# Performance work log

Measured on AMD Instinct MI355X. Metric: run time of the kernel, lower is better.

Reference implementation:

```python
import jax, jax.numpy as jnp
import numpy as np

N_BATCH = 4096
D_FEAT = 64
N_CLASSES = 10
DET_EPS = 1e-8


def setup_inputs() -> dict:
    key = jax.random.key(0)
    k1, k2, k3 = jax.random.split(key, 3)
    # small-magnitude means and variances bounded away from 0 keep the
    # KL values (and hence sigmoid(KL)) in a numerically meaningful range
    mu = jax.random.normal(k1, (N_BATCH, D_FEAT), dtype=jnp.float32) * 0.1
    var = jax.random.uniform(k2, (N_BATCH, D_FEAT), dtype=jnp.float32) + 0.5
    labels = jax.random.randint(k3, (N_BATCH,), 0, N_CLASSES)
    return {"mu": mu, "var": var, "labels": labels}


def _pairwise_kl(mu, var):
    """K[i, j] = KL(N(mu_i, diag(var_i)) || N(mu_j, diag(var_j))),
    matching the original's kl_mvn on the row/col tiling, but computed
    elementwise/matmul instead of dense diag_embed + inv/det (same math:
    inv(diag(S1)) @ diag(S0) summed == sum(S0/S1); det(diag(S)) == prod(S))."""
    D = mu.shape[1]
    inv_var = 1.0 / var                                   # [N, D]
    # tr term: sum_d var_i,d / var_j,d
    tr = var @ inv_var.T                                  # [N, N]
    # det term: det(S1)/ (det(S0)+eps) with diagonal determinants = products
    p = jnp.prod(var, axis=1)                             # [N]
    det = p[None, :] / (p[:, None] + DET_EPS)             # [N, N]
    # quad term: sum_d (mu_j - mu_i)^2 / var_j,d, expanded into matmuls
    mu_sq = mu * mu                                       # [N, D]
    quad = (mu_sq @ inv_var.T
            - 2.0 * (mu @ (mu * inv_var).T)
            + jnp.sum(mu_sq * inv_var, axis=1)[None, :])  # [N, N]
    return 0.5 * (tr + det + quad - D)


def reference(mu, var, labels):
    N = mu.shape[0]
    K = _pairwise_kl(mu, var)                 # KL(i -> j)
    sym = 0.5 * (K + K.T)                     # symmetric_kl over the pair grid
    logits = jax.nn.sigmoid(sym)              # [N, N]

    same = labels[:, None] == labels[None, :]
    off_diag = ~jnp.eye(N, dtype=bool)        # logits_mask: zero out diagonal
    p_mask = (same & off_diag).astype(logits.dtype)
    n_mask = ((~same) & off_diag).astype(logits.dtype)

    pos = logits * p_mask
    neg = logits * n_mask
    return (jnp.mean(pos), jnp.mean(neg), jnp.sum(pos), jnp.sum(neg))
```

## Files before the change

kernel.cpp:

```cpp
#include <hip/hip_runtime.h>


#define N 4096
#define D 64
#define KH 256
#define MT 128
#define TILES2 32
#define NBLK2 528
#define DET_EPS 1e-8f

typedef short bf16x8 __attribute__((ext_vector_type(8)));
typedef float f32x16 __attribute__((ext_vector_type(16)));

#define WS_H    0
#define WS_PSL  (N * KH * 2)
#define WS_PART (WS_PSL + N * 16)

static __device__ __forceinline__ unsigned short f2bf(float x) {
  unsigned int u = __float_as_uint(x);
  unsigned int r = (u + 0x7FFFu + ((u >> 16) & 1u)) >> 16;
  return (unsigned short)r;
}

static __device__ __forceinline__ f32x16 mfma_bf16(bf16x8 a, bf16x8 b, f32x16 c) {
  return __builtin_amdgcn_mfma_f32_32x32x16_bf16(a, b, c, 0, 0, 0);
}

__global__ __launch_bounds__(256) void precompute_kernel(
    const float* __restrict__ mu, const float* __restrict__ var,
    const int* __restrict__ labels,
    unsigned short* __restrict__ Hf, float4* __restrict__ PSL) {
  const int t = threadIdx.x;
  const int lane = t & 63;
  const int w = t >> 6;
  const int r = blockIdx.x * 4 + w;

  const float m = mu[r * D + lane];
  const float v = var[r * D + lane];
  const float g0 = 1.0f / v;
  const float f0 = v + m * m;
  const float f1 = -2.0f * m;
  const float g1 = m * g0;

  const size_t base = (size_t)(r >> 5) * 8192 + (size_t)(lane >> 2) * 512
                      + (size_t)(r & 31) * 16 + (size_t)(lane & 3) * 4;
  *(ushort4*)&Hf[base] = make_ushort4(f2bf(f0), f2bf(f1), f2bf(g0), f2bf(g1));

  float p = v;
  float s = m * m * g0;
  #pragma unroll
  for (int off = 1; off < 64; off <<= 1) {
    p *= __shfl_xor(p, off);
    s += __shfl_xor(s, off);
  }
  if (lane == 0) {
    PSL[r] = make_float4(p, 1.0f / (p + DET_EPS), 0.25f * s - 16.0f,
                         (float)labels[r]);
  }
}

__global__ __launch_bounds__(256, 2) void pair_kernel(
    const unsigned short* __restrict__ Hf,
    const float4* __restrict__ PSL, float* __restrict__ partial) {
  __shared__ float4 sPi[128];
  __shared__ float4 sPj[128];
  __shared__ float red[8];

  int L = (int)blockIdx.x;
  int it = (int)(32.5f - sqrtf(32.5f * 32.5f - 2.0f * (float)L));
  while (it > 0 && L < it * TILES2 - it * (it - 1) / 2) --it;
  while (L >= (it + 1) * TILES2 - (it + 1) * it / 2) ++it;
  const int jt = it + (L - (it * TILES2 - it * (it - 1) / 2));
  const int i0 = it * MT, j0 = jt * MT;

  const int t = threadIdx.x;
  const int lane = t & 63;
  const int w = t >> 6;
  const int sr = w >> 1, sc = w & 1;

  if (t < 128) sPi[t] = PSL[i0 + t];
  else sPj[t - 128] = PSL[j0 + t - 128];
  __syncthreads();

  const int l31 = lane & 31;
  const int slot = l31 * 16 + (lane >> 5) * 8;
  const unsigned short* pa = Hf + (size_t)(i0 / 32 + sr * 2) * 8192 + slot;
  const unsigned short* pb = Hf + (size_t)(j0 / 32 + sc * 2) * 8192 + slot;

  const bool active = !(it == jt && w == 2);

  f32x16 C00 = {}, C01 = {}, C10 = {}, C11 = {};
  float pos = 0.0f, neg = 0.0f;

  if (active) {
    #pragma unroll 4
    for (int k = 0; k < 16; ++k) {
      const bf16x8 a0 = *(const bf16x8*)(pa + k * 512);
      const bf16x8 a1 = *(const bf16x8*)(pa + 8192 + k * 512);
      const bf16x8 c0 = *(const bf16x8*)(pb + k * 512);
      const bf16x8 c1 = *(const bf16x8*)(pb + 8192 + k * 512);
      const bf16x8 b0 = __builtin_shufflevector(c0, c0, 2, 3, 0, 1, 6, 7, 4, 5);
      const bf16x8 b1 = __builtin_shufflevector(c1, c1, 2, 3, 0, 1, 6, 7, 4, 5);
      C00 = mfma_bf16(a0, b0, C00);
      C01 = mfma_bf16(a0, b1, C01);
      C10 = mfma_bf16(a1, b0, C10);
      C11 = mfma_bf16(a1, b1, C11);
    }

    const int rbase = 4 * (lane >> 5);
    #pragma unroll
    for (int mn = 0; mn < 4; ++mn) {
      const int m = mn >> 1, n = mn & 1;
      const f32x16 C = (mn == 0) ? C00 : (mn == 1) ? C01 : (mn == 2) ? C10 : C11;
      const int jloc = (sc * 2 + n) * 32 + l31;
      const int j = j0 + jloc;
      const float4 pj = sPj[jloc];
      #pragma unroll
      for (int r = 0; r < 16; ++r) {
        const int row = (r & 3) + 8 * (r >> 2) + rbase;
        const int iloc = (sr * 2 + m) * 32 + row;
        const int i = i0 + iloc;
        if (i < j) {
          const float4 pi = sPi[iloc];
          const float det = pj.x * pi.y + pi.x * pj.y;
          const float sym = 0.25f * (C[r] + det) + pi.z + pj.z;
          const float sig = __builtin_amdgcn_rcpf(1.0f + __expf(-sym));
          if (pi.w == pj.w) pos += sig; else neg += sig;
        }
      }
    }
  }

  #pragma unroll
  for (int off = 32; off > 0; off >>= 1) {
    pos += __shfl_down(pos, off);
    neg += __shfl_down(neg, off);
  }
  if (lane == 0) { red[w] = pos; red[4 + w] = neg; }
  __syncthreads();
  if (t == 0) {
    partial[L]         = red[0] + red[1] + red[2] + red[3];
    partial[NBLK2 + L] = red[4] + red[5] + red[6] + red[7];
  }
}

__global__ __launch_bounds__(256) void finalize_kernel(
    const float* __restrict__ partial, float* __restrict__ out) {
  __shared__ float redp[4], redn[4];
  const int t = threadIdx.x;
  const int lane = t & 63, w = t >> 6;
  float p = 0.0f, n = 0.0f;
  for (int i = t; i < NBLK2; i += 256) {
    p += partial[i];
    n += partial[NBLK2 + i];
  }
  #pragma unroll
  for (int off = 32; off > 0; off >>= 1) {
    p += __shfl_down(p, off);
    n += __shfl_down(n, off);
  }
  if (lane == 0) { redp[w] = p; redn[w] = n; }
  __syncthreads();
  if (t == 0) {
    const float pos = 2.0f * (redp[0] + redp[1] + redp[2] + redp[3]);
    const float neg = 2.0f * (redn[0] + redn[1] + redn[2] + redn[3]);
    out[0] = pos * (1.0f / 16777216.0f);
    out[1] = neg * (1.0f / 16777216.0f);
    out[2] = pos;
    out[3] = neg;
  }
}

extern "C" void kernel_launch(void* const* d_in, const int* in_sizes, int n_in,
                              void* d_out, int out_size, void* d_ws, size_t ws_size,
                              hipStream_t stream) {
  const float* mu = (const float*)d_in[0];
  const float* var = (const float*)d_in[1];
  const int* labels = (const int*)d_in[2];
  float* out = (float*)d_out;
  char* ws = (char*)d_ws;

  unsigned short* Hf = (unsigned short*)(ws + WS_H);
  float4* PSL = (float4*)(ws + WS_PSL);
  float* partial = (float*)(ws + WS_PART);

  precompute_kernel<<<dim3(N / 4), dim3(256), 0, stream>>>(mu, var, labels, Hf, PSL);
  pair_kernel<<<dim3(NBLK2), dim3(256), 0, stream>>>(Hf, PSL, partial);
  finalize_kernel<<<dim3(1), dim3(256), 0, stream>>>(partial, out);
}
```

Measured before the change: 78.68 us.

## Fuse precompute, pair and finalize into one cooperative kernel with grid syncs

Replaces the three launches with a single cooperative kernel of 512 blocks. Each block precomputes 8 rows, grid-syncs, then processes one off-diagonal tile or two diagonal tiles, grid-syncs again, and block 0 does the final reduction. The aim is to remove launch gaps and inter-kernel overhead, at the cost of two grid-wide barriers and some load imbalance, since the blocks that take two diagonal tiles do less work per tile. The original three-kernel path stays as a fallback if the cooperative launch fails.

```diff
diff --git a/kernel.cpp b/kernel.cpp
--- a/kernel.cpp
+++ b/kernel.cpp
@@ -1,4 +1,7 @@
 #include <hip/hip_runtime.h>
+#include <hip/hip_cooperative_groups.h>
+
+namespace cg = cooperative_groups;
 
 
 #define N 4096
@@ -6,7 +9,9 @@
 #define KH 256
 #define MT 128
 #define TILES2 32
+#define NOFF 496
 #define NBLK2 528
+#define GRID1 512
 #define DET_EPS 1e-8f
 
 typedef short bf16x8 __attribute__((ext_vector_type(8)));
@@ -26,15 +31,10 @@
   return __builtin_amdgcn_mfma_f32_32x32x16_bf16(a, b, c, 0, 0, 0);
 }
 
-__global__ __launch_bounds__(256) void precompute_kernel(
-    const float* __restrict__ mu, const float* __restrict__ var,
+static __device__ __forceinline__ void row_precompute(
+    int r, int lane, const float* __restrict__ mu, const float* __restrict__ var,
     const int* __restrict__ labels,
     unsigned short* __restrict__ Hf, float4* __restrict__ PSL) {
-  const int t = threadIdx.x;
-  const int lane = t & 63;
-  const int w = t >> 6;
-  const int r = blockIdx.x * 4 + w;
-
   const float m = mu[r * D + lane];
   const float v = var[r * D + lane];
   const float g0 = 1.0f / v;
@@ -59,33 +59,29 @@
   }
 }
 
-__global__ __launch_bounds__(256, 2) void pair_kernel(
+static __device__ __forceinline__ void do_tile(
+    int it, int jt, int slot,
     const unsigned short* __restrict__ Hf,
     const float4* __restrict__ PSL, float* __restrict__ partial) {
   __shared__ float4 sPi[128];
   __shared__ float4 sPj[128];
   __shared__ float red[8];
 
-  int L = (int)blockIdx.x;
-  int it = (int)(32.5f - sqrtf(32.5f * 32.5f - 2.0f * (float)L));
-  while (it > 0 && L < it * TILES2 - it * (it - 1) / 2) --it;
-  while (L >= (it + 1) * TILES2 - (it + 1) * it / 2) ++it;
-  const int jt = it + (L - (it * TILES2 - it * (it - 1) / 2));
   const int i0 = it * MT, j0 = jt * MT;
-
   const int t = threadIdx.x;
   const int lane = t & 63;
   const int w = t >> 6;
   const int sr = w >> 1, sc = w & 1;
 
+  __syncthreads();
   if (t < 128) sPi[t] = PSL[i0 + t];
   else sPj[t - 128] = PSL[j0 + t - 128];
   __syncthreads();
 
   const int l31 = lane & 31;
-  const int slot = l31 * 16 + (lane >> 5) * 8;
-  const unsigned short* pa = Hf + (size_t)(i0 / 32 + sr * 2) * 8192 + slot;
-  const unsigned short* pb = Hf + (size_t)(j0 / 32 + sc * 2) * 8192 + slot;
+  const int slot_f = l31 * 16 + (lane >> 5) * 8;
+  const unsigned short* pa = Hf + (size_t)(i0 / 32 + sr * 2) * 8192 + slot_f;
+  const unsigned short* pb = Hf + (size_t)(j0 / 32 + sc * 2) * 8192 + slot_f;
 
   const bool active = !(it == jt && w == 2);
 
@@ -139,9 +135,83 @@
   if (lane == 0) { red[w] = pos; red[4 + w] = neg; }
   __syncthreads();
   if (t == 0) {
-    partial[L]         = red[0] + red[1] + red[2] + red[3];
-    partial[NBLK2 + L] = red[4] + red[5] + red[6] + red[7];
-  }
+    partial[slot]         = red[0] + red[1] + red[2] + red[3];
+    partial[NBLK2 + slot] = red[4] + red[5] + red[6] + red[7];
+  }
+}
+
+__global__ __launch_bounds__(256, 2) void fused_kernel(
+    const float* __restrict__ mu, const float* __restrict__ var,
+    const int* __restrict__ labels,
+    unsigned short* __restrict__ Hf, float4* __restrict__ PSL,
+    float* __restrict__ partial, float* __restrict__ out) {
+  const int bid = (int)blockIdx.x;
+  const int t = (int)threadIdx.x;
+  const int lane = t & 63;
+  const int w = t >> 6;
+
+  #pragma unroll
+  for (int itr = 0; itr < 2; ++itr)
+    row_precompute(bid * 8 + itr * 4 + w, lane, mu, var, labels, Hf, PSL);
+
+  cg::this_grid().sync();
+
+  if (bid < NOFF) {
+    int it = (int)((63.0f - sqrtf(3969.0f - 8.0f * (float)bid)) * 0.5f);
+    while (it > 0 && bid < 31 * it - it * (it - 1) / 2) --it;
+    while (bid >= 31 * (it + 1) - (it + 1) * it / 2) ++it;
+    const int jt = it + 1 + (bid - (31 * it - it * (it - 1) / 2));
+    do_tile(it, jt, bid, Hf, PSL, partial);
+  } else {
+    const int dd = bid - NOFF;
+    do_tile(2 * dd,     2 * dd,     NOFF + 2 * dd,     Hf, PSL, partial);
+    do_tile(2 * dd + 1, 2 * dd + 1, NOFF + 2 * dd + 1, Hf, PSL, partial);
+  }
+
+  cg::this_grid().sync();
+
+  if (bid == 0) {
+    __shared__ float redp[4], redn[4];
+    float p = 0.0f, n = 0.0f;
+    for (int i = t; i < NBLK2; i += 256) {
+      p += partial[i];
+      n += partial[NBLK2 + i];
+    }
+    #pragma unroll
+    for (int off = 32; off > 0; off >>= 1) {
+      p += __shfl_down(p, off);
+      n += __shfl_down(n, off);
+    }
+    if (lane == 0) { redp[w] = p; redn[w] = n; }
+    __syncthreads();
+    if (t == 0) {
+      const float pos = 2.0f * (redp[0] + redp[1] + redp[2] + redp[3]);
+      const float neg = 2.0f * (redn[0] + redn[1] + redn[2] + redn[3]);
+      out[0] = pos * (1.0f / 16777216.0f);
+      out[1] = neg * (1.0f / 16777216.0f);
+      out[2] = pos;
+      out[3] = neg;
+    }
+  }
+}
+
+__global__ __launch_bounds__(256) void precompute_kernel(
+    const float* __restrict__ mu, const float* __restrict__ var,
+    const int* __restrict__ labels,
+    unsigned short* __restrict__ Hf, float4* __restrict__ PSL) {
+  const int t = threadIdx.x;
+  row_precompute(blockIdx.x * 4 + (t >> 6), t & 63, mu, var, labels, Hf, PSL);
+}
+
+__global__ __launch_bounds__(256, 2) void pair_kernel(
+    const unsigned short* __restrict__ Hf,
+    const float4* __restrict__ PSL, float* __restrict__ partial) {
+  int L = (int)blockIdx.x;
+  int it = (int)(32.5f - sqrtf(32.5f * 32.5f - 2.0f * (float)L));
+  while (it > 0 && L < it * TILES2 - it * (it - 1) / 2) --it;
+  while (L >= (it + 1) * TILES2 - (it + 1) * it / 2) ++it;
+  const int jt = it + (L - (it * TILES2 - it * (it - 1) / 2));
+  do_tile(it, jt, L, Hf, PSL, partial);
 }
 
 __global__ __launch_bounds__(256) void finalize_kernel(
@@ -184,7 +254,14 @@
   float4* PSL = (float4*)(ws + WS_PSL);
   float* partial = (float*)(ws + WS_PART);
 
-  precompute_kernel<<<dim3(N / 4), dim3(256), 0, stream>>>(mu, var, labels, Hf, PSL);
-  pair_kernel<<<dim3(NBLK2), dim3(256), 0, stream>>>(Hf, PSL, partial);
-  finalize_kernel<<<dim3(1), dim3(256), 0, stream>>>(partial, out);
-}
+  void* args[] = {(void*)&mu, (void*)&var, (void*)&labels,
+                  (void*)&Hf, (void*)&PSL, (void*)&partial, (void*)&out};
+  hipError_t e = hipLaunchCooperativeKernel((const void*)fused_kernel,
+                                            dim3(GRID1), dim3(256), args, 0,
+                                            stream);
+  if (e != hipSuccess) {
+    precompute_kernel<<<dim3(N / 4), dim3(256), 0, stream>>>(mu, var, labels, Hf, PSL);
+    pair_kernel<<<dim3(NBLK2), dim3(256), 0, stream>>>(Hf, PSL, partial);
+    finalize_kernel<<<dim3(1), dim3(256), 0, stream>>>(partial, out);
+  }
+}
```

After: 207.8 us. 164% more time.

## Fuse finalize into pair kernel via last-block reduction and pack diagonal tiles

Applied to the files above, without the earlier changes.

Removes the separate finalize launch: each pair block publishes its partials, bumps an atomic counter reset by the precompute kernel, and the last block to finish does the final reduction. The grid also shrinks from 528 to 512 blocks, with 496 off-diagonal tiles at one per block and the 32 diagonal tiles paired two per block. The diagonal masking becomes a compile-time template specialization. The goal is to drop one launch and even out per-block work, at the cost of atomics, a threadfence, and serial diagonal tiles in the last 16 blocks.

```diff
diff --git a/kernel.cpp b/kernel.cpp
--- a/kernel.cpp
+++ b/kernel.cpp
@@ -6,7 +6,9 @@
 #define KH 256
 #define MT 128
 #define TILES2 32
+#define NOFF 496
 #define NBLK2 528
+#define GRID2 512
 #define DET_EPS 1e-8f
 
 typedef short bf16x8 __attribute__((ext_vector_type(8)));
@@ -15,6 +17,7 @@
 #define WS_H    0
 #define WS_PSL  (N * KH * 2)
 #define WS_PART (WS_PSL + N * 16)
+#define WS_CNT  (WS_PART + 2 * NBLK2 * 4)
 
 static __device__ __forceinline__ unsigned short f2bf(float x) {
   unsigned int u = __float_as_uint(x);
@@ -29,11 +32,14 @@
 __global__ __launch_bounds__(256) void precompute_kernel(
     const float* __restrict__ mu, const float* __restrict__ var,
     const int* __restrict__ labels,
-    unsigned short* __restrict__ Hf, float4* __restrict__ PSL) {
+    unsigned short* __restrict__ Hf, float4* __restrict__ PSL,
+    unsigned int* __restrict__ counter) {
   const int t = threadIdx.x;
   const int lane = t & 63;
   const int w = t >> 6;
   const int r = blockIdx.x * 4 + w;
+
+  if (blockIdx.x == 0 && t == 0) *counter = 0u;
 
   const float m = mu[r * D + lane];
   const float v = var[r * D + lane];
@@ -59,35 +65,29 @@
   }
 }
 
-__global__ __launch_bounds__(256, 2) void pair_kernel(
+template <bool DIAG>
+static __device__ __forceinline__ void do_tile(
+    int it, int jt, int slot,
     const unsigned short* __restrict__ Hf,
-    const float4* __restrict__ PSL, float* __restrict__ partial) {
-  __shared__ float4 sPi[128];
-  __shared__ float4 sPj[128];
-  __shared__ float red[8];
-
-  int L = (int)blockIdx.x;
-  int it = (int)(32.5f - sqrtf(32.5f * 32.5f - 2.0f * (float)L));
-  while (it > 0 && L < it * TILES2 - it * (it - 1) / 2) --it;
-  while (L >= (it + 1) * TILES2 - (it + 1) * it / 2) ++it;
-  const int jt = it + (L - (it * TILES2 - it * (it - 1) / 2));
+    const float4* __restrict__ PSL, float* __restrict__ partial,
+    float4* sPi, float4* sPj, float* red) {
   const int i0 = it * MT, j0 = jt * MT;
-
   const int t = threadIdx.x;
   const int lane = t & 63;
   const int w = t >> 6;
   const int sr = w >> 1, sc = w & 1;
 
+  __syncthreads();
   if (t < 128) sPi[t] = PSL[i0 + t];
   else sPj[t - 128] = PSL[j0 + t - 128];
   __syncthreads();
 
   const int l31 = lane & 31;
-  const int slot = l31 * 16 + (lane >> 5) * 8;
-  const unsigned short* pa = Hf + (size_t)(i0 / 32 + sr * 2) * 8192 + slot;
-  const unsigned short* pb = Hf + (size_t)(j0 / 32 + sc * 2) * 8192 + slot;
-
-  const bool active = !(it == jt && w == 2);
+  const int slot_f = l31 * 16 + (lane >> 5) * 8;
+  const unsigned short* pa = Hf + (size_t)(i0 / 32 + sr * 2) * 8192 + slot_f;
+  const unsigned short* pb = Hf + (size_t)(j0 / 32 + sc * 2) * 8192 + slot_f;
+
+  const bool active = !(DIAG && w == 2);
 
   f32x16 C00 = {}, C01 = {}, C10 = {}, C11 = {};
   float pos = 0.0f, neg = 0.0f;
@@ -113,14 +113,12 @@
       const int m = mn >> 1, n = mn & 1;
       const f32x16 C = (mn == 0) ? C00 : (mn == 1) ? C01 : (mn == 2) ? C10 : C11;
       const int jloc = (sc * 2 + n) * 32 + l31;
-      const int j = j0 + jloc;
       const float4 pj = sPj[jloc];
       #pragma unroll
       for (int r = 0; r < 16; ++r) {
         const int row = (r & 3) + 8 * (r >> 2) + rbase;
         const int iloc = (sr * 2 + m) * 32 + row;
-        const int i = i0 + iloc;
-        if (i < j) {
+        if (!DIAG || (i0 + iloc) < (j0 + jloc)) {
           const float4 pi = sPi[iloc];
           const float det = pj.x * pi.y + pi.x * pj.y;
           const float sym = 0.25f * (C[r] + det) + pi.z + pj.z;
@@ -139,35 +137,63 @@
   if (lane == 0) { red[w] = pos; red[4 + w] = neg; }
   __syncthreads();
   if (t == 0) {
-    partial[L]         = red[0] + red[1] + red[2] + red[3];
-    partial[NBLK2 + L] = red[4] + red[5] + red[6] + red[7];
-  }
-}
-
-__global__ __launch_bounds__(256) void finalize_kernel(
-    const float* __restrict__ partial, float* __restrict__ out) {
-  __shared__ float redp[4], redn[4];
-  const int t = threadIdx.x;
-  const int lane = t & 63, w = t >> 6;
-  float p = 0.0f, n = 0.0f;
-  for (int i = t; i < NBLK2; i += 256) {
-    p += partial[i];
-    n += partial[NBLK2 + i];
-  }
-  #pragma unroll
-  for (int off = 32; off > 0; off >>= 1) {
-    p += __shfl_down(p, off);
-    n += __shfl_down(n, off);
-  }
-  if (lane == 0) { redp[w] = p; redn[w] = n; }
-  __syncthreads();
-  if (t == 0) {
-    const float pos = 2.0f * (redp[0] + redp[1] + redp[2] + redp[3]);
-    const float neg = 2.0f * (redn[0] + redn[1] + redn[2] + redn[3]);
-    out[0] = pos * (1.0f / 16777216.0f);
-    out[1] = neg * (1.0f / 16777216.0f);
-    out[2] = pos;
-    out[3] = neg;
+    atomicExch(&partial[slot],         red[0] + red[1] + red[2] + red[3]);
+    atomicExch(&partial[NBLK2 + slot], red[4] + red[5] + red[6] + red[7]);
+  }
+}
+
+__global__ __launch_bounds__(256, 2) void pair_finalize_kernel(
+    const unsigned short* __restrict__ Hf,
+    const float4* __restrict__ PSL, float* __restrict__ partial,
+    unsigned int* __restrict__ counter, float* __restrict__ out) {
+  __shared__ float4 sPi[128];
+  __shared__ float4 sPj[128];
+  __shared__ float red[8];
+  __shared__ unsigned int sOrd;
+
+  const int bid = (int)blockIdx.x;
+  const int t = (int)threadIdx.x;
+
+  if (bid < NOFF) {
+    int it = (int)((63.0f - sqrtf(3969.0f - 8.0f * (float)bid)) * 0.5f);
+    while (it > 0 && bid < 31 * it - it * (it - 1) / 2) --it;
+    while (bid >= 31 * (it + 1) - (it + 1) * it / 2) ++it;
+    const int jt = it + 1 + (bid - (31 * it - it * (it - 1) / 2));
+    do_tile<false>(it, jt, bid, Hf, PSL, partial, sPi, sPj, red);
+  } else {
+    const int dd = bid - NOFF;
+    do_tile<true>(2 * dd,     2 * dd,     NOFF + 2 * dd,     Hf, PSL, partial,
+                  sPi, sPj, red);
+    do_tile<true>(2 * dd + 1, 2 * dd + 1, NOFF + 2 * dd + 1, Hf, PSL, partial,
+                  sPi, sPj, red);
+  }
+
+  __threadfence();
+  if (t == 0) sOrd = atomicAdd(counter, 1u);
+  __syncthreads();
+  if (sOrd == GRID2 - 1) {
+    __shared__ float redp[4], redn[4];
+    const int lane = t & 63, w = t >> 6;
+    float p = 0.0f, n = 0.0f;
+    for (int i = t; i < NBLK2; i += 256) {
+      p += atomicAdd(&partial[i], 0.0f);
+      n += atomicAdd(&partial[NBLK2 + i], 0.0f);
+    }
+    #pragma unroll
+    for (int off = 32; off > 0; off >>= 1) {
+      p += __shfl_down(p, off);
+      n += __shfl_down(n, off);
+    }
+    if (lane == 0) { redp[w] = p; redn[w] = n; }
+    __syncthreads();
+    if (t == 0) {
+      const float pos = 2.0f * (redp[0] + redp[1] + redp[2] + redp[3]);
+      const float neg = 2.0f * (redn[0] + redn[1] + redn[2] + redn[3]);
+      out[0] = pos * (1.0f / 16777216.0f);
+      out[1] = neg * (1.0f / 16777216.0f);
+      out[2] = pos;
+      out[3] = neg;
+    }
   }
 }
 
@@ -183,8 +209,10 @@
   unsigned short* Hf = (unsigned short*)(ws + WS_H);
   float4* PSL = (float4*)(ws + WS_PSL);
   float* partial = (float*)(ws + WS_PART);
-
-  precompute_kernel<<<dim3(N / 4), dim3(256), 0, stream>>>(mu, var, labels, Hf, PSL);
-  pair_kernel<<<dim3(NBLK2), dim3(256), 0, stream>>>(Hf, PSL, partial);
-  finalize_kernel<<<dim3(1), dim3(256), 0, stream>>>(partial, out);
-}
+  unsigned int* counter = (unsigned int*)(ws + WS_CNT);
+
+  precompute_kernel<<<dim3(N / 4), dim3(256), 0, stream>>>(mu, var, labels, Hf,
+                                                           PSL, counter);
+  pair_finalize_kernel<<<dim3(GRID2), dim3(256), 0, stream>>>(Hf, PSL, partial,
+                                                              counter, out);
+}
```

Result: slower. 107.7 us (+36.9%).

## Switch pair kernel to single-wave 64x64 triangular tiles with prefetched loads

Applied to the files above, without the earlier changes.

Replaces the 256-thread, 128x128 upper-triangle tile blocks with 2080 one-wavefront blocks, each handling a 64x64 tile. Each wave writes its partial sums directly, so the shared-memory cross-wave reduction and its barrier go away. The diagonal-tile masking is specialised via a template, and the k-loop now prefetches the next iteration's operands into registers. The aim is finer load balance across CUs and less idle work on diagonal tiles. The cost is more blocks, more repeated PSL loads, and a larger partial array for finalize to sum.

```diff
diff --git a/kernel.cpp b/kernel.cpp
--- a/kernel.cpp
+++ b/kernel.cpp
@@ -4,9 +4,9 @@
 #define N 4096
 #define D 64
 #define KH 256
-#define MT 128
-#define TILES2 32
-#define NBLK2 528
+#define MT 64
+#define TILES 64
+#define NT 2080
 #define DET_EPS 1e-8f
 
 typedef short bf16x8 __attribute__((ext_vector_type(8)));
@@ -59,74 +59,74 @@
   }
 }
 
-__global__ __launch_bounds__(256, 2) void pair_kernel(
+template <bool DIAG>
+static __device__ __forceinline__ void tile64(
+    int it, int jt, int slot,
     const unsigned short* __restrict__ Hf,
-    const float4* __restrict__ PSL, float* __restrict__ partial) {
-  __shared__ float4 sPi[128];
-  __shared__ float4 sPj[128];
-  __shared__ float red[8];
-
-  int L = (int)blockIdx.x;
-  int it = (int)(32.5f - sqrtf(32.5f * 32.5f - 2.0f * (float)L));
-  while (it > 0 && L < it * TILES2 - it * (it - 1) / 2) --it;
-  while (L >= (it + 1) * TILES2 - (it + 1) * it / 2) ++it;
-  const int jt = it + (L - (it * TILES2 - it * (it - 1) / 2));
+    const float4* __restrict__ PSL, float* __restrict__ partial,
+    float4* sPi, float4* sPj) {
   const int i0 = it * MT, j0 = jt * MT;
-
-  const int t = threadIdx.x;
-  const int lane = t & 63;
-  const int w = t >> 6;
-  const int sr = w >> 1, sc = w & 1;
-
-  if (t < 128) sPi[t] = PSL[i0 + t];
-  else sPj[t - 128] = PSL[j0 + t - 128];
+  const int lane = (int)threadIdx.x & 63;
+  const int l31 = lane & 31;
+
+  sPi[lane] = PSL[i0 + lane];
+  sPj[lane] = PSL[j0 + lane];
   __syncthreads();
 
-  const int l31 = lane & 31;
-  const int slot = l31 * 16 + (lane >> 5) * 8;
-  const unsigned short* pa = Hf + (size_t)(i0 / 32 + sr * 2) * 8192 + slot;
-  const unsigned short* pb = Hf + (size_t)(j0 / 32 + sc * 2) * 8192 + slot;
-
-  const bool active = !(it == jt && w == 2);
+  const int slot_f = l31 * 16 + (lane >> 5) * 8;
+  const unsigned short* pa = Hf + (size_t)(i0 >> 5) * 8192 + slot_f;
+  const unsigned short* pb = Hf + (size_t)(j0 >> 5) * 8192 + slot_f;
+
+#define LDA0(k) (*(const bf16x8*)(pa + (k) * 512))
+#define LDA1(k) (*(const bf16x8*)(pa + 8192 + (k) * 512))
+#define LDB0(k) (*(const bf16x8*)(pb + (k) * 512))
+#define LDB1(k) (*(const bf16x8*)(pb + 8192 + (k) * 512))
+#define PI(x) __builtin_shufflevector((x), (x), 2, 3, 0, 1, 6, 7, 4, 5)
 
   f32x16 C00 = {}, C01 = {}, C10 = {}, C11 = {};
+
+  bf16x8 a0x = LDA0(0), a1x = LDA1(0), b0x = LDB0(0), b1x = LDB1(0);
+  #pragma unroll
+  for (int k = 0; k < 16; ++k) {
+    bf16x8 a0y, a1y, b0y, b1y;
+    if (k < 15) {
+      a0y = LDA0(k + 1); a1y = LDA1(k + 1);
+      b0y = LDB0(k + 1); b1y = LDB1(k + 1);
+    }
+    const bf16x8 p0 = PI(b0x), p1 = PI(b1x);
+    C00 = mfma_bf16(a0x, p0, C00);
+    C01 = mfma_bf16(a0x, p1, C01);
+    C10 = mfma_bf16(a1x, p0, C10);
+    C11 = mfma_bf16(a1x, p1, C11);
+    if (k < 15) {
+      a0x = a0y; a1x = a1y; b0x = b0y; b1x = b1y;
+    }
+  }
+#undef LDA0
+#undef LDA1
+#undef LDB0
+#undef LDB1
+#undef PI
+
+  const int rbase = 4 * (lane >> 5);
   float pos = 0.0f, neg = 0.0f;
-
-  if (active) {
-    #pragma unroll 4
-    for (int k = 0; k < 16; ++k) {
-      const bf16x8 a0 = *(const bf16x8*)(pa + k * 512);
-      const bf16x8 a1 = *(const bf16x8*)(pa + 8192 + k * 512);
-      const bf16x8 c0 = *(const bf16x8*)(pb + k * 512);
-      const bf16x8 c1 = *(const bf16x8*)(pb + 8192 + k * 512);
-      const bf16x8 b0 = __builtin_shufflevector(c0, c0, 2, 3, 0, 1, 6, 7, 4, 5);
-      const bf16x8 b1 = __builtin_shufflevector(c1, c1, 2, 3, 0, 1, 6, 7, 4, 5);
-      C00 = mfma_bf16(a0, b0, C00);
-      C01 = mfma_bf16(a0, b1, C01);
-      C10 = mfma_bf16(a1, b0, C10);
-      C11 = mfma_bf16(a1, b1, C11);
-    }
-
-    const int rbase = 4 * (lane >> 5);
+  #pragma unroll
+  for (int mn = 0; mn < 4; ++mn) {
+    const int m = mn >> 1, n = mn & 1;
+    if (DIAG && m == 1 && n == 0) continue;
+    const f32x16 C = (mn == 0) ? C00 : (mn == 1) ? C01 : (mn == 2) ? C10 : C11;
+    const int jloc = n * 32 + l31;
+    const float4 pj = sPj[jloc];
     #pragma unroll
-    for (int mn = 0; mn < 4; ++mn) {
-      const int m = mn >> 1, n = mn & 1;
-      const f32x16 C = (mn == 0) ? C00 : (mn == 1) ? C01 : (mn == 2) ? C10 : C11;
-      const int jloc = (sc * 2 + n) * 32 + l31;
-      const int j = j0 + jloc;
-      const float4 pj = sPj[jloc];
-      #pragma unroll
-      for (int r = 0; r < 16; ++r) {
-        const int row = (r & 3) + 8 * (r >> 2) + rbase;
-        const int iloc = (sr * 2 + m) * 32 + row;
-        const int i = i0 + iloc;
-        if (i < j) {
-          const float4 pi = sPi[iloc];
-          const float det = pj.x * pi.y + pi.x * pj.y;
-          const float sym = 0.25f * (C[r] + det) + pi.z + pj.z;
-          const float sig = __builtin_amdgcn_rcpf(1.0f + __expf(-sym));
-          if (pi.w == pj.w) pos += sig; else neg += sig;
-        }
+    for (int r = 0; r < 16; ++r) {
+      const int row = (r & 3) + 8 * (r >> 2) + rbase;
+      const int iloc = m * 32 + row;
+      if (!DIAG || (i0 + iloc) < (j0 + jloc)) {
+        const float4 pi = sPi[iloc];
+        const float det = pj.x * pi.y + pi.x * pj.y;
+        const float sym = 0.25f * (C[r] + det) + pi.z + pj.z;
+        const float sig = __builtin_amdgcn_rcpf(1.0f + __expf(-sym));
+        if (pi.w == pj.w) pos += sig; else neg += sig;
       }
     }
   }
@@ -136,12 +136,26 @@
     pos += __shfl_down(pos, off);
     neg += __shfl_down(neg, off);
   }
-  if (lane == 0) { red[w] = pos; red[4 + w] = neg; }
-  __syncthreads();
-  if (t == 0) {
-    partial[L]         = red[0] + red[1] + red[2] + red[3];
-    partial[NBLK2 + L] = red[4] + red[5] + red[6] + red[7];
-  }
+  if (lane == 0) {
+    partial[slot]      = pos;
+    partial[NT + slot] = neg;
+  }
+}
+
+__global__ __launch_bounds__(64, 4) void pair64_kernel(
+    const unsigned short* __restrict__ Hf,
+    const float4* __restrict__ PSL, float* __restrict__ partial) {
+  __shared__ float4 sPi[64];
+  __shared__ float4 sPj[64];
+
+  int L = (int)blockIdx.x;
+  int it = (int)((129.0f - sqrtf(16641.0f - 8.0f * (float)L)) * 0.5f);
+  while (it > 0 && L < it * TILES - it * (it - 1) / 2) --it;
+  while (L >= (it + 1) * TILES - (it + 1) * it / 2) ++it;
+  const int jt = it + (L - (it * TILES - it * (it - 1) / 2));
+
+  if (it == jt) tile64<true>(it, jt, L, Hf, PSL, partial, sPi, sPj);
+  else          tile64<false>(it, jt, L, Hf, PSL, partial, sPi, sPj);
 }
 
 __global__ __launch_bounds__(256) void finalize_kernel(
@@ -150,9 +164,9 @@
   const int t = threadIdx.x;
   const int lane = t & 63, w = t >> 6;
   float p = 0.0f, n = 0.0f;
-  for (int i = t; i < NBLK2; i += 256) {
+  for (int i = t; i < NT; i += 256) {
     p += partial[i];
-    n += partial[NBLK2 + i];
+    n += partial[NT + i];
   }
   #pragma unroll
   for (int off = 32; off > 0; off >>= 1) {
@@ -185,6 +199,6 @@
   float* partial = (float*)(ws + WS_PART);
 
   precompute_kernel<<<dim3(N / 4), dim3(256), 0, stream>>>(mu, var, labels, Hf, PSL);
-  pair_kernel<<<dim3(NBLK2), dim3(256), 0, stream>>>(Hf, PSL, partial);
+  pair64_kernel<<<dim3(NT), dim3(64), 0, stream>>>(Hf, PSL, partial);
   finalize_kernel<<<dim3(1), dim3(256), 0, stream>>>(partial, out);
 }
```

Result: slower. 90.35 us (+14.8%).
